# Kernel tuning notes

Hardware: AMD Instinct MI355X
Metric: run time of the kernel (lower is better)

Reference implementation:

```python
import jax, jax.numpy as jnp
import numpy as np

B, S, H = 2, 2048, 1024
NH = 16
HD = H // NH
SCALE = 1.0 / np.sqrt(HD).astype(np.float32)


def setup_inputs() -> dict:
    key = jax.random.key(0)
    ks = jax.random.split(key, 7)
    lim = 1.0 / np.sqrt(H)  # lecun-ish init scale for linear weights
    return {
        "query": jax.random.normal(ks[0], (B, S, H), dtype=jnp.float32),
        "key_in": jax.random.normal(ks[1], (B, S, H), dtype=jnp.float32),
        "value": jax.random.normal(ks[2], (B, S, H), dtype=jnp.float32),
        "attention_mask": jnp.ones((B, S), dtype=jnp.int32),
        "Wq": jax.random.uniform(ks[3], (H, H), jnp.float32, -lim, lim),
        "Wk": jax.random.uniform(ks[4], (H, H), jnp.float32, -lim, lim),
        "Wv": jax.random.uniform(ks[5], (H, H), jnp.float32, -lim, lim),
        "Wo": jax.random.uniform(ks[6], (H, H), jnp.float32, -lim, lim),
    }


def reference(query, key_in, value, attention_mask, Wq, Wk, Wv, Wo):
    b, s, _ = query.shape
    # projections (no bias)
    q = (query @ Wq).reshape(b, s, NH, HD).transpose(0, 2, 1, 3)  # [b,h,s,d]
    k = (key_in @ Wk).reshape(b, s, NH, HD).transpose(0, 2, 1, 3)
    v = (value @ Wv).reshape(b, s, NH, HD).transpose(0, 2, 1, 3)

    scores = jnp.einsum("bhqd,bhkd->bhqk", q, k) * SCALE  # [b,h,s,s]
    mask = attention_mask[:, None, None, :]  # broadcast over heads & query pos
    scores = jnp.where(mask == 0, -1e9, scores)
    attn = jax.nn.softmax(scores, axis=-1)

    ctx = jnp.einsum("bhqk,bhkd->bhqd", attn, v)
    ctx = ctx.transpose(0, 2, 1, 3).reshape(b, s, H)
    out = ctx @ Wo
    return out, jnp.mean(attn, axis=1)
```

## Files before the change

### kernel.cpp

```cpp
#include <hip/hip_runtime.h>
#include <stdint.h>

#define BB 2
#define SS 2048
#define HH 1024
#define NHEAD 16
#define HDIM 64

constexpr int   BSROWS = BB * SS;
constexpr float SCALE  = 0.125f;
constexpr float LOG2E  = 1.4426950408889634f;
constexpr float SL     = SCALE * LOG2E;

typedef __bf16 bf16;
typedef __attribute__((ext_vector_type(8))) __bf16 bf16x8;
typedef __attribute__((ext_vector_type(4))) __bf16 bf16x4;
typedef __attribute__((ext_vector_type(4))) float  f32x4;

#define MFMA16(a, b, c) __builtin_amdgcn_mfma_f32_16x16x32_bf16((a), (b), (c), 0, 0, 0)

__device__ __forceinline__ void gload_lds16(const void* g, void* l) {
  __builtin_amdgcn_global_load_lds((const __attribute__((address_space(1))) void*)g,
                                   (__attribute__((address_space(3))) void*)l, 16, 0, 0);
}

__global__ __launch_bounds__(256) void cvt_in(const float* __restrict__ q, const float* __restrict__ k,
                                              const float* __restrict__ v, const int* __restrict__ mask,
                                              bf16* __restrict__ xq, bf16* __restrict__ xk,
                                              bf16* __restrict__ xv, float* __restrict__ bias2) {
  int i = blockIdx.x * 256 + threadIdx.x;
  int e = i * 4;
  f32x4 a = *(const f32x4*)(q + e);
  f32x4 b = *(const f32x4*)(k + e);
  f32x4 c = *(const f32x4*)(v + e);
  *(bf16x4*)(xq + e) = __builtin_convertvector(a, bf16x4);
  *(bf16x4*)(xk + e) = __builtin_convertvector(b, bf16x4);
  *(bf16x4*)(xv + e) = __builtin_convertvector(c, bf16x4);
  if (i < BB * SS) bias2[i] = mask[i] ? 0.0f : -1e9f * LOG2E;
}

__global__ __launch_bounds__(256) void cvt_wt(const float* __restrict__ Wq, const float* __restrict__ Wk,
                                              const float* __restrict__ Wv, const float* __restrict__ Wo,
                                              bf16* __restrict__ Wt) {
  __shared__ float tile[32][33];
  int z = blockIdx.z;
  const float* W = (z == 0) ? Wq : (z == 1) ? Wk : (z == 2) ? Wv : Wo;
  bf16* out = Wt + (size_t)z * HH * HH;
  int bx = blockIdx.x * 32, by = blockIdx.y * 32;
  int tx = threadIdx.x, ty = threadIdx.y;
#pragma unroll
  for (int j = 0; j < 32; j += 8)
    tile[ty + j][tx] = W[(size_t)(by + ty + j) * HH + bx + tx];
  __syncthreads();
#pragma unroll
  for (int j = 0; j < 32; j += 8)
    out[(size_t)(bx + ty + j) * HH + by + tx] = (bf16)tile[tx][ty + j];
}

__global__ __launch_bounds__(256) void gemm128(const bf16* __restrict__ Abase, const bf16* __restrict__ Btbase,
                                               bf16* __restrict__ Qo, bf16* __restrict__ Ko,
                                               bf16* __restrict__ Vto, float* __restrict__ outF, int mode) {
  int id  = blockIdx.x + 8 * blockIdx.y + 256 * blockIdx.z;
  int nwg = 256 * gridDim.z;
  int sw  = (id & 7) * (nwg >> 3) + (id >> 3);
  int bx  = sw & 7, by = (sw >> 3) & 31, bz = sw >> 8;

  int zmode = (mode < 0) ? bz : mode;
  const bf16* A  = Abase  + (mode < 0 ? (size_t)bz * BSROWS * HH : 0);
  const bf16* Bt = Btbase + (mode < 0 ? (size_t)bz * HH * HH : 0);

  __shared__ __align__(16) bf16 lA[2][128 * 32];
  __shared__ __align__(16) bf16 lB[2][128 * 32];

  int t = threadIdx.x;
  int w = t >> 6, l = t & 63, lg = l >> 4, lr = l & 15;
  int m0 = by * 128, n0 = bx * 128;
  int wr = (w >> 1) * 64, wc = (w & 1) * 64;

  f32x4 zero4 = {0.f, 0.f, 0.f, 0.f};
  f32x4 acc[4][4];
#pragma unroll
  for (int i = 0; i < 4; i++)
#pragma unroll
    for (int j = 0; j < 4; j++) acc[i][j] = zero4;

#pragma unroll
  for (int i = 0; i < 2; i++) {
    int idx = i * 256 + t;
    gload_lds16(A  + (size_t)(m0 + (idx >> 2)) * HH + (idx & 3) * 8, &lA[0][(i * 256 + w * 64) * 8]);
    gload_lds16(Bt + (size_t)(n0 + (idx >> 2)) * HH + (idx & 3) * 8, &lB[0][(i * 256 + w * 64) * 8]);
  }
  __syncthreads();

  for (int kt = 0; kt < 32; kt++) {
    int cur = kt & 1;
    if (kt < 31) {
      int kn = (kt + 1) * 32;
#pragma unroll
      for (int i = 0; i < 2; i++) {
        int idx = i * 256 + t;
        gload_lds16(A  + (size_t)(m0 + (idx >> 2)) * HH + kn + (idx & 3) * 8, &lA[cur ^ 1][(i * 256 + w * 64) * 8]);
        gload_lds16(Bt + (size_t)(n0 + (idx >> 2)) * HH + kn + (idx & 3) * 8, &lB[cur ^ 1][(i * 256 + w * 64) * 8]);
      }
    }
    bf16x8 af[4], bq[4];
#pragma unroll
    for (int mi = 0; mi < 4; mi++) af[mi] = *(const bf16x8*)&lA[cur][(wr + mi * 16 + lr) * 32 + lg * 8];
#pragma unroll
    for (int ni = 0; ni < 4; ni++) bq[ni] = *(const bf16x8*)&lB[cur][(wc + ni * 16 + lr) * 32 + lg * 8];
#pragma unroll
    for (int mi = 0; mi < 4; mi++)
#pragma unroll
      for (int ni = 0; ni < 4; ni++)
        acc[mi][ni] = MFMA16(af[mi], bq[ni], acc[mi][ni]);
    __syncthreads();
  }

#pragma unroll
  for (int mi = 0; mi < 4; mi++) {
    int row0 = m0 + wr + mi * 16 + lg * 4;
#pragma unroll
    for (int ni = 0; ni < 4; ni++) {
      int col = n0 + wc + ni * 16 + lr;
      if (zmode == 3) {
#pragma unroll
        for (int r = 0; r < 4; r++) outF[(size_t)(row0 + r) * HH + col] = acc[mi][ni][r];
      } else if (zmode == 2) {
        int b = row0 >> 11, s0 = row0 & (SS - 1);
        int h = col >> 6, d = col & 63;
        bf16x4 pk;
#pragma unroll
        for (int r = 0; r < 4; r++) pk[r] = (bf16)acc[mi][ni][r];
        *(bf16x4*)&Vto[((size_t)(b * NHEAD + h) * HDIM + d) * SS + s0] = pk;
      } else {
        bf16* dst = (zmode == 0) ? Qo : Ko;
        int h = col >> 6, d = col & 63;
#pragma unroll
        for (int r = 0; r < 4; r++) {
          int row = row0 + r;
          int b = row >> 11, s = row & (SS - 1);
          dst[((size_t)(b * NHEAD + h) * SS + s) * HDIM + d] = (bf16)acc[mi][ni][r];
        }
      }
    }
  }
}

__global__ __launch_bounds__(256, 2) void attn_pv(const bf16* __restrict__ Q, const bf16* __restrict__ K,
                                                  const bf16* __restrict__ Vt, const float* __restrict__ bias2,
                                                  float* __restrict__ invl, bf16* __restrict__ ctx) {
  int id = blockIdx.x + 16 * blockIdx.y + 256 * blockIdx.z;
  int sw = (id & 7) * 64 + (id >> 3);
  int b = sw >> 8, h = (sw >> 4) & 15, q0 = (sw & 15) * 128;
  int t = threadIdx.x, w = t >> 6, l = t & 63, lg = l >> 4, lr = l & 15;
  size_t hb = ((size_t)b * NHEAD + h) * SS;
  const bf16* Qh = Q + hb * HDIM;
  const bf16* Kh = K + hb * HDIM;
  const bf16* Vh = Vt + ((size_t)b * NHEAD + h) * HDIM * SS;
  const float* biasb = bias2 + b * SS;

  __shared__ __align__(16) bf16 sK[2][64][72];
  __shared__ __align__(16) bf16 sV[2][64][72];
  __shared__ __align__(16) bf16 lp[4][32][72];

  int r0 = t >> 3, c0 = (t & 7) * 8;
  bf16x8 kreg[2], vreg[2];

  int qa = q0 + w * 32;
  int rowa = qa + lr, rowb = qa + 16 + lr;
  bf16x8 qf0a = *(const bf16x8*)&Qh[(size_t)rowa * HDIM + lg * 8];
  bf16x8 qf1a = *(const bf16x8*)&Qh[(size_t)rowa * HDIM + 32 + lg * 8];
  bf16x8 qf0b = *(const bf16x8*)&Qh[(size_t)rowb * HDIM + lg * 8];
  bf16x8 qf1b = *(const bf16x8*)&Qh[(size_t)rowb * HDIM + 32 + lg * 8];

  f32x4 zero4 = {0.f, 0.f, 0.f, 0.f};
  f32x4 lacca = zero4, laccb = zero4;
  f32x4 ctxa[4], ctxb[4];
#pragma unroll
  for (int nd = 0; nd < 4; nd++) { ctxa[nd] = zero4; ctxb[nd] = zero4; }

#pragma unroll
  for (int i = 0; i < 2; i++) {
    int row = i * 32 + r0;
    kreg[i] = *(const bf16x8*)&Kh[(size_t)row * HDIM + c0];
    vreg[i] = *(const bf16x8*)&Vh[(size_t)row * SS + c0];
  }
#pragma unroll
  for (int i = 0; i < 2; i++) {
    int row = i * 32 + r0;
    *(bf16x8*)&sK[0][row][c0] = kreg[i];
    *(bf16x8*)&sV[0][row][c0] = vreg[i];
  }
  __syncthreads();

  for (int kt = 0; kt < 32; kt++) {
    int k0 = kt * 64, cur = kt & 1;
    if (kt < 31) {
      int kn = k0 + 64;
#pragma unroll
      for (int i = 0; i < 2; i++) {
        int row = i * 32 + r0;
        kreg[i] = *(const bf16x8*)&Kh[(size_t)(kn + row) * HDIM + c0];
        vreg[i] = *(const bf16x8*)&Vh[(size_t)row * SS + kn + c0];
      }
    }
    f32x4 acca[4], accb[4];
#pragma unroll
    for (int ni = 0; ni < 4; ni++) {
      const bf16* kp = &sK[cur][ni * 16 + lr][lg * 8];
      bf16x8 kf0 = *(const bf16x8*)kp;
      bf16x8 kf1 = *(const bf16x8*)(kp + 32);
      acca[ni] = MFMA16(kf1, qf1a, MFMA16(kf0, qf0a, zero4));
      accb[ni] = MFMA16(kf1, qf1b, MFMA16(kf0, qf0b, zero4));
    }
    f32x4 pa4[4], pb4[4];
#pragma unroll
    for (int ni = 0; ni < 4; ni++) {
      f32x4 bv = *(const f32x4*)&biasb[k0 + ni * 16 + lg * 4];
      f32x4 za = acca[ni] * SL + bv;
      f32x4 zb = accb[ni] * SL + bv;
#pragma unroll
      for (int r = 0; r < 4; r++) {
        pa4[ni][r] = __builtin_amdgcn_exp2f(za[r]);
        pb4[ni][r] = __builtin_amdgcn_exp2f(zb[r]);
      }
    }
    lacca += (pa4[0] + pa4[1]) + (pa4[2] + pa4[3]);
    laccb += (pb4[0] + pb4[1]) + (pb4[2] + pb4[3]);
#pragma unroll
    for (int ni = 0; ni < 4; ni++) {
      *(bf16x4*)&lp[w][lr][ni * 16 + lg * 4]      = __builtin_convertvector(pa4[ni], bf16x4);
      *(bf16x4*)&lp[w][16 + lr][ni * 16 + lg * 4] = __builtin_convertvector(pb4[ni], bf16x4);
    }
#pragma unroll
    for (int kk = 0; kk < 2; kk++) {
      bf16x8 paa = *(const bf16x8*)&lp[w][lr][kk * 32 + lg * 8];
      bf16x8 pab = *(const bf16x8*)&lp[w][16 + lr][kk * 32 + lg * 8];
#pragma unroll
      for (int nd = 0; nd < 4; nd++) {
        bf16x8 vf = *(const bf16x8*)&sV[cur][nd * 16 + lr][kk * 32 + lg * 8];
        ctxa[nd] = MFMA16(paa, vf, ctxa[nd]);
        ctxb[nd] = MFMA16(pab, vf, ctxb[nd]);
      }
    }
    if (kt < 31) {
#pragma unroll
      for (int i = 0; i < 2; i++) {
        int row = i * 32 + r0;
        *(bf16x8*)&sK[cur ^ 1][row][c0] = kreg[i];
        *(bf16x8*)&sV[cur ^ 1][row][c0] = vreg[i];
      }
      __syncthreads();
    }
  }

  float lsa = (lacca[0] + lacca[1]) + (lacca[2] + lacca[3]);
  float lsb = (laccb[0] + laccb[1]) + (laccb[2] + laccb[3]);
  lsa += __shfl_xor(lsa, 16); lsa += __shfl_xor(lsa, 32);
  lsb += __shfl_xor(lsb, 16); lsb += __shfl_xor(lsb, 32);
  float ila = 1.0f / lsa, ilb = 1.0f / lsb;
  f32x4 ilva, ilvb;
#pragma unroll
  for (int r = 0; r < 4; r++) { ilva[r] = __shfl(ila, lg * 4 + r); ilvb[r] = __shfl(ilb, lg * 4 + r); }
#pragma unroll
  for (int nd = 0; nd < 4; nd++)
#pragma unroll
    for (int r = 0; r < 4; r++) {
      int ra = qa + lg * 4 + r, rb = qa + 16 + lg * 4 + r;
      ctx[(size_t)(b * SS + ra) * HH + h * HDIM + nd * 16 + lr] = (bf16)(ctxa[nd][r] * ilva[r]);
      ctx[(size_t)(b * SS + rb) * HH + h * HDIM + nd * 16 + lr] = (bf16)(ctxb[nd][r] * ilvb[r]);
    }
  if (l < 16) {
    invl[hb + qa + l]      = ila;
    invl[hb + qa + 16 + l] = ilb;
  }
}

__global__ __launch_bounds__(256, 4) void attn_mean(const bf16* __restrict__ Q, const bf16* __restrict__ K,
                                                    const float* __restrict__ bias2,
                                                    const float* __restrict__ invl, float* __restrict__ meanOut) {
  int id = blockIdx.x + 16 * blockIdx.y + 512 * blockIdx.z;
  int sw = (id & 7) * 128 + (id >> 3);
  int b = sw >> 9, kc0 = ((sw >> 4) & 31) * 64, q0 = (sw & 15) * 128;
  int t = threadIdx.x, w = t >> 6, l = t & 63, lg = l >> 4, lr = l & 15;
  const float* biasb = bias2 + b * SS;
  __shared__ __align__(16) bf16 sK[2][64][64];

  int rloc = l >> 3;
  int csw  = (l & 7) ^ (rloc & 7);
  int swz  = lr & 7;

  int qa = q0 + w * 32;
  int rowa = qa + lr, rowb = qa + 16 + lr;

  f32x4 bv[4];
#pragma unroll
  for (int ni = 0; ni < 4; ni++) bv[ni] = *(const f32x4*)&biasb[kc0 + ni * 16 + lg * 4];

  f32x4 zero4 = {0.f, 0.f, 0.f, 0.f};
  f32x4 macca[4], maccb[4];
#pragma unroll
  for (int ni = 0; ni < 4; ni++) { macca[ni] = zero4; maccb[ni] = zero4; }

  bf16x8 qf0a, qf1a, qf0b, qf1b;
  float ila, ilb;
  {
    const bf16* Kh0 = K + ((size_t)b * NHEAD) * SS * HDIM;
#pragma unroll
    for (int i = 0; i < 2; i++) {
      int rs = w * 16 + i * 8;
      gload_lds16(Kh0 + (size_t)(kc0 + rs + rloc) * HDIM + csw * 8, &sK[0][rs][0]);
    }
    const bf16* Qh0 = Q + ((size_t)b * NHEAD) * SS * HDIM;
    qf0a = *(const bf16x8*)&Qh0[(size_t)rowa * HDIM + lg * 8];
    qf1a = *(const bf16x8*)&Qh0[(size_t)rowa * HDIM + 32 + lg * 8];
    qf0b = *(const bf16x8*)&Qh0[(size_t)rowb * HDIM + lg * 8];
    qf1b = *(const bf16x8*)&Qh0[(size_t)rowb * HDIM + 32 + lg * 8];
    size_t hb0 = (size_t)b * NHEAD * SS;
    ila = invl[hb0 + rowa] * (1.0f / NHEAD);
    ilb = invl[hb0 + rowb] * (1.0f / NHEAD);
  }
  __syncthreads();

  for (int h = 0; h < NHEAD; h++) {
    int cur = h & 1;
    bf16x8 qn0a, qn1a, qn0b, qn1b;
    float ina = 0.f, inb = 0.f;
    if (h < NHEAD - 1) {
      size_t hbn = ((size_t)b * NHEAD + h + 1) * SS;
      const bf16* Khn = K + hbn * HDIM;
#pragma unroll
      for (int i = 0; i < 2; i++) {
        int rs = w * 16 + i * 8;
        gload_lds16(Khn + (size_t)(kc0 + rs + rloc) * HDIM + csw * 8, &sK[cur ^ 1][rs][0]);
      }
      const bf16* Qhn = Q + hbn * HDIM;
      qn0a = *(const bf16x8*)&Qhn[(size_t)rowa * HDIM + lg * 8];
      qn1a = *(const bf16x8*)&Qhn[(size_t)rowa * HDIM + 32 + lg * 8];
      qn0b = *(const bf16x8*)&Qhn[(size_t)rowb * HDIM + lg * 8];
      qn1b = *(const bf16x8*)&Qhn[(size_t)rowb * HDIM + 32 + lg * 8];
      ina = invl[hbn + rowa] * (1.0f / NHEAD);
      inb = invl[hbn + rowb] * (1.0f / NHEAD);
    }
#pragma unroll
    for (int ni = 0; ni < 4; ni++) {
      bf16x8 kf0 = *(const bf16x8*)&sK[cur][ni * 16 + lr][(lg ^ swz) * 8];
      bf16x8 kf1 = *(const bf16x8*)&sK[cur][ni * 16 + lr][((4 + lg) ^ swz) * 8];
      f32x4 acca = MFMA16(kf1, qf1a, MFMA16(kf0, qf0a, zero4));
      f32x4 accb = MFMA16(kf1, qf1b, MFMA16(kf0, qf0b, zero4));
      f32x4 za = acca * SL + bv[ni];
      f32x4 zb = accb * SL + bv[ni];
#pragma unroll
      for (int r = 0; r < 4; r++) {
        macca[ni][r] += __builtin_amdgcn_exp2f(za[r]) * ila;
        maccb[ni][r] += __builtin_amdgcn_exp2f(zb[r]) * ilb;
      }
    }
    if (h < NHEAD - 1) {
      qf0a = qn0a; qf1a = qn1a; qf0b = qn0b; qf1b = qn1b;
      ila = ina; ilb = inb;
      __syncthreads();
    }
  }
  float* meanB = meanOut + (size_t)b * SS * SS;
#pragma unroll
  for (int ni = 0; ni < 4; ni++) {
    *(f32x4*)&meanB[(size_t)rowa * SS + kc0 + ni * 16 + lg * 4] = macca[ni];
    *(f32x4*)&meanB[(size_t)rowb * SS + kc0 + ni * 16 + lg * 4] = maccb[ni];
  }
}

extern "C" void kernel_launch(void* const* d_in, const int* in_sizes, int n_in,
                              void* d_out, int out_size, void* d_ws, size_t ws_size,
                              hipStream_t stream) {
  const float* query  = (const float*)d_in[0];
  const float* key_in = (const float*)d_in[1];
  const float* value  = (const float*)d_in[2];
  const int*   mask   = (const int*)d_in[3];
  const float* Wq     = (const float*)d_in[4];
  const float* Wk     = (const float*)d_in[5];
  const float* Wv     = (const float*)d_in[6];
  const float* Wo     = (const float*)d_in[7];

  char* ws = (char*)d_ws;
  bf16*  Xb    = (bf16*)(ws);
  bf16*  Wt    = (bf16*)(ws + 25165824);
  bf16*  Qb    = (bf16*)(ws + 33554432);
  bf16*  Kb    = (bf16*)(ws + 41943040);
  bf16*  Vtb   = (bf16*)(ws + 50331648);
  float* invlb = (float*)(ws + 58982400);
  float* biasb = (float*)(ws + 59244544);
  bf16*  ctxb  = Xb;

  float* outF  = (float*)d_out;
  float* meanF = outF + (size_t)BB * SS * HH;

  cvt_in<<<4096, 256, 0, stream>>>(query, key_in, value, mask,
                                   Xb, Xb + 4194304, Xb + 8388608, biasb);
  cvt_wt<<<dim3(32, 32, 4), dim3(32, 8), 0, stream>>>(Wq, Wk, Wv, Wo, Wt);
  gemm128<<<dim3(8, 32, 3), 256, 0, stream>>>(Xb, Wt, Qb, Kb, Vtb, nullptr, -1);
  attn_pv<<<dim3(16, 16, 2), 256, 0, stream>>>(Qb, Kb, Vtb, biasb, invlb, ctxb);
  attn_mean<<<dim3(16, 32, 2), 256, 0, stream>>>(Qb, Kb, biasb, invlb, meanF);
  gemm128<<<dim3(8, 32, 1), 256, 0, stream>>>(ctxb, Wt + 3 * (size_t)HH * HH,
                                              nullptr, nullptr, nullptr, outF, 3);
}
```

Measured before the change: 180.3 us.

## Software-pipeline PV MFMA one tile behind QK and softmax in attn_pv

Splits the attention inner loop so that each iteration runs the P·V MFMAs for the previous key tile before the QK MFMAs and exp of the current tile. V fragments are copied to registers and P is double-buffered in LDS, so the next tile's shared buffers can be overwritten safely. The aim is to overlap MFMA work with the exp/convert VALU work and hide the LDS round-trip latency on P. In exchange it adds 8 bf16x8 registers per thread plus double the LDS for P, which could reduce occupancy below the 2-blocks target.

```diff
diff --git a/kernel.cpp b/kernel.cpp
--- a/kernel.cpp
+++ b/kernel.cpp
@@ -161,7 +161,7 @@
 
   __shared__ __align__(16) bf16 sK[2][64][72];
   __shared__ __align__(16) bf16 sV[2][64][72];
-  __shared__ __align__(16) bf16 lp[4][32][72];
+  __shared__ __align__(16) bf16 lp[4][2][32][72];
 
   int r0 = t >> 3, c0 = (t & 7) * 8;
   bf16x8 kreg[2], vreg[2];
@@ -178,6 +178,7 @@
   f32x4 ctxa[4], ctxb[4];
 #pragma unroll
   for (int nd = 0; nd < 4; nd++) { ctxa[nd] = zero4; ctxb[nd] = zero4; }
+  bf16x8 vh[2][4];
 
 #pragma unroll
   for (int i = 0; i < 2; i++) {
@@ -194,7 +195,7 @@
   __syncthreads();
 
   for (int kt = 0; kt < 32; kt++) {
-    int k0 = kt * 64, cur = kt & 1;
+    int k0 = kt * 64, cur = kt & 1, prev = cur ^ 1;
     if (kt < 31) {
       int kn = k0 + 64;
 #pragma unroll
@@ -202,6 +203,18 @@
         int row = i * 32 + r0;
         kreg[i] = *(const bf16x8*)&Kh[(size_t)(kn + row) * HDIM + c0];
         vreg[i] = *(const bf16x8*)&Vh[(size_t)row * SS + kn + c0];
+      }
+    }
+    if (kt > 0) {
+#pragma unroll
+      for (int kk = 0; kk < 2; kk++) {
+        bf16x8 paa = *(const bf16x8*)&lp[w][prev][lr][kk * 32 + lg * 8];
+        bf16x8 pab = *(const bf16x8*)&lp[w][prev][16 + lr][kk * 32 + lg * 8];
+#pragma unroll
+        for (int nd = 0; nd < 4; nd++) {
+          ctxa[nd] = MFMA16(paa, vh[kk][nd], ctxa[nd]);
+          ctxb[nd] = MFMA16(pab, vh[kk][nd], ctxb[nd]);
+        }
       }
     }
     f32x4 acca[4], accb[4];
@@ -213,6 +226,11 @@
       acca[ni] = MFMA16(kf1, qf1a, MFMA16(kf0, qf0a, zero4));
       accb[ni] = MFMA16(kf1, qf1b, MFMA16(kf0, qf0b, zero4));
     }
+#pragma unroll
+    for (int kk = 0; kk < 2; kk++)
+#pragma unroll
+      for (int nd = 0; nd < 4; nd++)
+        vh[kk][nd] = *(const bf16x8*)&sV[cur][nd * 16 + lr][kk * 32 + lg * 8];
     f32x4 pa4[4], pb4[4];
 #pragma unroll
     for (int ni = 0; ni < 4; ni++) {
@@ -229,28 +247,28 @@
     laccb += (pb4[0] + pb4[1]) + (pb4[2] + pb4[3]);
 #pragma unroll
     for (int ni = 0; ni < 4; ni++) {
-      *(bf16x4*)&lp[w][lr][ni * 16 + lg * 4]      = __builtin_convertvector(pa4[ni], bf16x4);
-      *(bf16x4*)&lp[w][16 + lr][ni * 16 + lg * 4] = __builtin_convertvector(pb4[ni], bf16x4);
-    }
-#pragma unroll
-    for (int kk = 0; kk < 2; kk++) {
-      bf16x8 paa = *(const bf16x8*)&lp[w][lr][kk * 32 + lg * 8];
-      bf16x8 pab = *(const bf16x8*)&lp[w][16 + lr][kk * 32 + lg * 8];
-#pragma unroll
-      for (int nd = 0; nd < 4; nd++) {
-        bf16x8 vf = *(const bf16x8*)&sV[cur][nd * 16 + lr][kk * 32 + lg * 8];
-        ctxa[nd] = MFMA16(paa, vf, ctxa[nd]);
-        ctxb[nd] = MFMA16(pab, vf, ctxb[nd]);
-      }
+      *(bf16x4*)&lp[w][cur][lr][ni * 16 + lg * 4]      = __builtin_convertvector(pa4[ni], bf16x4);
+      *(bf16x4*)&lp[w][cur][16 + lr][ni * 16 + lg * 4] = __builtin_convertvector(pb4[ni], bf16x4);
     }
     if (kt < 31) {
 #pragma unroll
       for (int i = 0; i < 2; i++) {
         int row = i * 32 + r0;
-        *(bf16x8*)&sK[cur ^ 1][row][c0] = kreg[i];
-        *(bf16x8*)&sV[cur ^ 1][row][c0] = vreg[i];
+        *(bf16x8*)&sK[prev][row][c0] = kreg[i];
+        *(bf16x8*)&sV[prev][row][c0] = vreg[i];
       }
       __syncthreads();
+    }
+  }
+
+#pragma unroll
+  for (int kk = 0; kk < 2; kk++) {
+    bf16x8 paa = *(const bf16x8*)&lp[w][1][lr][kk * 32 + lg * 8];
+    bf16x8 pab = *(const bf16x8*)&lp[w][1][16 + lr][kk * 32 + lg * 8];
+#pragma unroll
+    for (int nd = 0; nd < 4; nd++) {
+      ctxa[nd] = MFMA16(paa, vh[kk][nd], ctxa[nd]);
+      ctxb[nd] = MFMA16(pab, vh[kk][nd], ctxb[nd]);
     }
   }
 
```

After: 178.6 us. Within noise of the previous version (-0.9%).
